# Optimization experiments

Measured on AMD Instinct MI355X. Metric: run time of the kernel, lower is better.

The kernel has to match this reference:

```python
import jax, jax.numpy as jnp
import numpy as np

BASE_T = 0.07
ALPHA = 0.5
EPS = 1e-12  # torch F.normalize eps


def _l2_normalize(x):
    norm = jnp.linalg.norm(x, axis=1, keepdims=True)
    return x / jnp.maximum(norm, EPS)


def setup_inputs() -> dict:
    key = jax.random.key(0)
    k1, k2, k3 = jax.random.split(key, 3)
    B, D, H, W = 4096, 512, 16, 16
    return {
        "emb1": jax.random.normal(k1, (B, D), dtype=jnp.float32),
        "emb2": jax.random.normal(k2, (B, D), dtype=jnp.float32),
        "attention_map": jax.random.uniform(k3, (B, H, W), dtype=jnp.float32),
    }


def reference(emb1, emb2, attention_map):
    B = emb1.shape[0]
    e1 = _l2_normalize(emb1)
    e2 = _l2_normalize(emb2)

    att = attention_map.mean(axis=(1, 2))                     # [B]
    temp = (BASE_T * (1.0 + ALPHA * att))[:, None]            # [B, 1]

    x = jnp.concatenate([e1, e2], axis=0)                     # [2B, D]
    x_swap = jnp.concatenate([e2, e1], axis=0)                # [2B, D]
    temp_cat = jnp.concatenate([temp, temp], axis=0)          # [2B, 1]

    sim = jnp.matmul(x, x.T) / temp_cat                       # [2B, 2B]
    pos_sim = jnp.sum(x * x_swap, axis=1) / temp_cat[:, 0]    # [2B]

    diag = jnp.eye(2 * B, dtype=bool)
    sim = jnp.where(diag, -jnp.inf, sim)                      # exp(-inf) = 0

    denominator = jnp.exp(sim).sum(axis=1)                    # [2B]
    loss = -jnp.log(jnp.exp(pos_sim) / denominator)
    return loss.mean()
```

## Files before the change

### kernel.cpp

```cpp
#include <hip/hip_runtime.h>
#include <hip/hip_bf16.h>
#include <math.h>

#define B_ROWS 4096
#define D_DIM 512
#define TWO_B 8192
#define HW_N 256
#define BASE_T 0.07f
#define ALPHA_C 0.5f
#define LOG2E 1.44269504088896340736f

typedef __bf16 v8bf __attribute__((ext_vector_type(8)));
typedef float v4f __attribute__((ext_vector_type(4)));

__device__ __forceinline__ float fast_exp2(float x) {
#if __has_builtin(__builtin_amdgcn_exp2f)
    return __builtin_amdgcn_exp2f(x);
#else
    return exp2f(x);
#endif
}

__global__ __launch_bounds__(256) void prep_kernel(
    const float* __restrict__ emb1, const float* __restrict__ emb2,
    const float* __restrict__ att, __hip_bfloat16* __restrict__ X,
    float* __restrict__ inv_temp, float* __restrict__ pos)
{
    const int b = blockIdx.x;
    const int t = threadIdx.x;
    const float* e1 = emb1 + (size_t)b * D_DIM;
    const float* e2 = emb2 + (size_t)b * D_DIM;
    float a1 = e1[t], c1 = e1[t + 256];
    float a2 = e2[t], c2 = e2[t + 256];
    float av = att[(size_t)b * HW_N + t];
    float s1 = a1 * a1 + c1 * c1;
    float s2 = a2 * a2 + c2 * c2;
    float s12 = a1 * a2 + c1 * c2;
    #pragma unroll
    for (int m = 1; m < 64; m <<= 1) {
        s1  += __shfl_xor(s1, m, 64);
        s2  += __shfl_xor(s2, m, 64);
        s12 += __shfl_xor(s12, m, 64);
        av  += __shfl_xor(av, m, 64);
    }
    __shared__ float red[4][4];
    const int w = t >> 6, lane = t & 63;
    if (lane == 0) { red[w][0] = s1; red[w][1] = s2; red[w][2] = s12; red[w][3] = av; }
    __syncthreads();
    const float T1  = red[0][0] + red[1][0] + red[2][0] + red[3][0];
    const float T2  = red[0][1] + red[1][1] + red[2][1] + red[3][1];
    const float T12 = red[0][2] + red[1][2] + red[2][2] + red[3][2];
    const float Ta  = red[0][3] + red[1][3] + red[2][3] + red[3][3];
    const float i1 = 1.0f / fmaxf(sqrtf(T1), 1e-12f);
    const float i2 = 1.0f / fmaxf(sqrtf(T2), 1e-12f);
    const float it = 1.0f / (BASE_T * (1.0f + ALPHA_C * (Ta * (1.0f / 256.0f))));
    __hip_bfloat16* x1 = X + (size_t)b * D_DIM;
    __hip_bfloat16* x2 = X + (size_t)(b + B_ROWS) * D_DIM;
    x1[t]       = __float2bfloat16(a1 * i1);
    x1[t + 256] = __float2bfloat16(c1 * i1);
    x2[t]       = __float2bfloat16(a2 * i2);
    x2[t + 256] = __float2bfloat16(c2 * i2);
    if (t == 0) {
        inv_temp[b] = it * LOG2E;
        inv_temp[b + B_ROWS] = it * LOG2E;
        pos[b] = (T12 * i1 * i2) * it;
    }
}

__device__ __forceinline__ void gload_lds16(const void* g, void* s) {
    __builtin_amdgcn_global_load_lds(
        (const __attribute__((address_space(1))) unsigned int*)g,
        (__attribute__((address_space(3))) unsigned int*)s,
        16, 0, 0);
}

__global__ __launch_bounds__(256) void gram_kernel(
    const __hip_bfloat16* __restrict__ X,
    const float* __restrict__ inv_temp,
    float* __restrict__ partial)
{
    const int bid = blockIdx.x;
    int rb = (int)((129.0f - sqrtf(129.0f * 129.0f - 8.0f * (float)bid)) * 0.5f);
    rb = rb < 0 ? 0 : (rb > 63 ? 63 : rb);
    while (rb > 0 && (rb * (129 - rb)) / 2 > bid) rb--;
    while (rb < 63 && ((rb + 1) * (129 - (rb + 1))) / 2 <= bid) rb++;
    const int cb = rb + (bid - (rb * (129 - rb)) / 2);

    __shared__ __hip_bfloat16 smA[128 * 128];
    __shared__ __hip_bfloat16 smB[128 * 128];

    const int rowBase = rb * 128;
    const int colBase = cb * 128;

    const int tid  = threadIdx.x;
    const int w    = tid >> 6;
    const int lane = tid & 63;
    const int quad = lane >> 4;
    const int t    = lane & 15;
    const int wm   = w >> 1;
    const int wn   = w & 1;

    const int srow   = lane >> 4;
    const int schunk = lane & 15;

    v4f acc[4][4];
    #pragma unroll
    for (int a = 0; a < 4; a++)
        #pragma unroll
        for (int b2 = 0; b2 < 4; b2++)
            acc[a][b2] = v4f{0.0f, 0.0f, 0.0f, 0.0f};

    const __hip_bfloat16* Arow0 = X + (size_t)rowBase * D_DIM;
    const __hip_bfloat16* Brow0 = X + (size_t)colBase * D_DIM;

    for (int kk = 0; kk < D_DIM; kk += 128) {
        #pragma unroll
        for (int j = 0; j < 8; j++) {
            const int g = w * 8 + j;
            const int r = g * 4 + srow;
            const int gc = schunk ^ (r & 15);
            gload_lds16(Arow0 + (size_t)r * D_DIM + kk + gc * 8,
                        &smA[g * 512]);
            gload_lds16(Brow0 + (size_t)r * D_DIM + kk + gc * 8,
                        &smB[g * 512]);
        }
        __syncthreads();

        #pragma unroll
        for (int s = 0; s < 4; s++) {
            v8bf af[4], bf[4];
            #pragma unroll
            for (int mi = 0; mi < 4; mi++) {
                const int row = wm * 64 + mi * 16 + t;
                const int p = (s * 4 + quad) ^ t;
                af[mi] = *(const v8bf*)&smA[row * 128 + p * 8];
            }
            #pragma unroll
            for (int ni = 0; ni < 4; ni++) {
                const int col = wn * 64 + ni * 16 + t;
                const int p = (s * 4 + quad) ^ t;
                bf[ni] = *(const v8bf*)&smB[col * 128 + p * 8];
            }
            #pragma unroll
            for (int mi = 0; mi < 4; mi++)
                #pragma unroll
                for (int ni = 0; ni < 4; ni++)
                    acc[mi][ni] = __builtin_amdgcn_mfma_f32_16x16x32_bf16(
                        af[mi], bf[ni], acc[mi][ni], 0, 0, 0);
        }
        __syncthreads();
    }

    v4f itv[4];
    #pragma unroll
    for (int mi = 0; mi < 4; mi++)
        itv[mi] = *(const v4f*)&inv_temp[rowBase + wm * 64 + mi * 16 + quad * 4];

    float* prow = partial + (size_t)(cb * 2 + wn) * TWO_B;
    #pragma unroll
    for (int mi = 0; mi < 4; mi++) {
        #pragma unroll
        for (int r = 0; r < 4; r++) {
            const int i = rowBase + wm * 64 + mi * 16 + quad * 4 + r;
            const float it = itv[mi][r];
            float s = 0.0f;
            #pragma unroll
            for (int ni = 0; ni < 4; ni++) {
                const int j = colBase + wn * 64 + ni * 16 + t;
                const float v = fast_exp2(acc[mi][ni][r] * it);
                s += (i == j) ? 0.0f : v;
            }
            s += __shfl_xor(s, 1, 64);
            s += __shfl_xor(s, 2, 64);
            s += __shfl_xor(s, 4, 64);
            s += __shfl_xor(s, 8, 64);
            if (t == 0) prow[i] = s;
        }
    }

    if (rb != cb) {
        float itj[4];
        float cs[4] = {0.0f, 0.0f, 0.0f, 0.0f};
        #pragma unroll
        for (int ni = 0; ni < 4; ni++)
            itj[ni] = inv_temp[colBase + wn * 64 + ni * 16 + t];
        #pragma unroll
        for (int mi = 0; mi < 4; mi++)
            #pragma unroll
            for (int r = 0; r < 4; r++)
                #pragma unroll
                for (int ni = 0; ni < 4; ni++)
                    cs[ni] += fast_exp2(acc[mi][ni][r] * itj[ni]);
        float* pcol = partial + (size_t)(rb * 2 + wm) * TWO_B;
        #pragma unroll
        for (int ni = 0; ni < 4; ni++) {
            cs[ni] += __shfl_xor(cs[ni], 16, 64);
            cs[ni] += __shfl_xor(cs[ni], 32, 64);
            if (quad == 0) pcol[colBase + wn * 64 + ni * 16 + t] = cs[ni];
        }
    }
}

__global__ __launch_bounds__(256) void finish1(
    const float* __restrict__ partial, const float* __restrict__ pos,
    float* __restrict__ blockSums)
{
    const int i = blockIdx.x * 256 + threadIdx.x;
    float d = 0.0f;
    #pragma unroll 8
    for (int s = 0; s < 128; s++) d += partial[(size_t)s * TWO_B + i];
    float li = logf(d) - pos[i & (B_ROWS - 1)];
    #pragma unroll
    for (int m = 1; m < 64; m <<= 1) li += __shfl_xor(li, m, 64);
    __shared__ float red[4];
    const int w = threadIdx.x >> 6, lane = threadIdx.x & 63;
    if (lane == 0) red[w] = li;
    __syncthreads();
    if (threadIdx.x == 0) blockSums[blockIdx.x] = red[0] + red[1] + red[2] + red[3];
}

__global__ void finish2(const float* __restrict__ blockSums, float* __restrict__ out)
{
    const int lane = threadIdx.x;
    float v = (lane < 32) ? blockSums[lane] : 0.0f;
    #pragma unroll
    for (int m = 1; m < 64; m <<= 1) v += __shfl_xor(v, m, 64);
    if (lane == 0) out[0] = v * (1.0f / 8192.0f);
}

extern "C" void kernel_launch(void* const* d_in, const int* in_sizes, int n_in,
                              void* d_out, int out_size, void* d_ws, size_t ws_size,
                              hipStream_t stream) {
    const float* emb1 = (const float*)d_in[0];
    const float* emb2 = (const float*)d_in[1];
    const float* att  = (const float*)d_in[2];
    float* out = (float*)d_out;

    char* ws = (char*)d_ws;
    __hip_bfloat16* X  = (__hip_bfloat16*)ws;
    float* inv_temp    = (float*)(ws + 8388608);
    float* pos         = (float*)(ws + 8388608 + 32768);
    float* partial     = (float*)(ws + 8388608 + 32768 + 16384);
    float* blockSums   = (float*)(ws + 8388608 + 32768 + 16384 + 4194304);

    prep_kernel<<<B_ROWS, 256, 0, stream>>>(emb1, emb2, att, X, inv_temp, pos);
    gram_kernel<<<2080, 256, 0, stream>>>(X, inv_temp, partial);
    finish1<<<TWO_B / 256, 256, 0, stream>>>(partial, pos, blockSums);
    finish2<<<1, 64, 0, stream>>>(blockSums, out);
}
```

Before: 143.4 us.

## Switch Gram matrix to FP8 MFMA with FP8 normalized embeddings

Normalized embeddings are now stored as packed FP8 instead of bf16, which halves workspace traffic, and the Gram kernel uses fp8 16x16x32 MFMA instructions with 256-byte K tiles, so there are two K iterations instead of four. The prep kernel loads float2 per thread, and the gram block index is permuted across groups of eight for a different schedule over the triangular tiles. The aim is to cut memory and MFMA cost, at the price of much lower precision in the similarity logits. Those logits are divided by a temperature near 0.07 and exponentiated, so the loss may drift from the reference.

```diff
diff --git a/kernel.cpp b/kernel.cpp
--- a/kernel.cpp
+++ b/kernel.cpp
@@ -10,7 +10,6 @@
 #define ALPHA_C 0.5f
 #define LOG2E 1.44269504088896340736f
 
-typedef __bf16 v8bf __attribute__((ext_vector_type(8)));
 typedef float v4f __attribute__((ext_vector_type(4)));
 
 __device__ __forceinline__ float fast_exp2(float x) {
@@ -23,19 +22,17 @@
 
 __global__ __launch_bounds__(256) void prep_kernel(
     const float* __restrict__ emb1, const float* __restrict__ emb2,
-    const float* __restrict__ att, __hip_bfloat16* __restrict__ X,
+    const float* __restrict__ att, unsigned short* __restrict__ X8,
     float* __restrict__ inv_temp, float* __restrict__ pos)
 {
     const int b = blockIdx.x;
     const int t = threadIdx.x;
-    const float* e1 = emb1 + (size_t)b * D_DIM;
-    const float* e2 = emb2 + (size_t)b * D_DIM;
-    float a1 = e1[t], c1 = e1[t + 256];
-    float a2 = e2[t], c2 = e2[t + 256];
+    const float2 a1 = ((const float2*)(emb1 + (size_t)b * D_DIM))[t];
+    const float2 a2 = ((const float2*)(emb2 + (size_t)b * D_DIM))[t];
     float av = att[(size_t)b * HW_N + t];
-    float s1 = a1 * a1 + c1 * c1;
-    float s2 = a2 * a2 + c2 * c2;
-    float s12 = a1 * a2 + c1 * c2;
+    float s1  = a1.x * a1.x + a1.y * a1.y;
+    float s2  = a2.x * a2.x + a2.y * a2.y;
+    float s12 = a1.x * a2.x + a1.y * a2.y;
     #pragma unroll
     for (int m = 1; m < 64; m <<= 1) {
         s1  += __shfl_xor(s1, m, 64);
@@ -54,12 +51,10 @@
     const float i1 = 1.0f / fmaxf(sqrtf(T1), 1e-12f);
     const float i2 = 1.0f / fmaxf(sqrtf(T2), 1e-12f);
     const float it = 1.0f / (BASE_T * (1.0f + ALPHA_C * (Ta * (1.0f / 256.0f))));
-    __hip_bfloat16* x1 = X + (size_t)b * D_DIM;
-    __hip_bfloat16* x2 = X + (size_t)(b + B_ROWS) * D_DIM;
-    x1[t]       = __float2bfloat16(a1 * i1);
-    x1[t + 256] = __float2bfloat16(c1 * i1);
-    x2[t]       = __float2bfloat16(a2 * i2);
-    x2[t + 256] = __float2bfloat16(c2 * i2);
+    const int p1 = __builtin_amdgcn_cvt_pk_fp8_f32(a1.x * i1, a1.y * i1, 0, false);
+    const int p2 = __builtin_amdgcn_cvt_pk_fp8_f32(a2.x * i2, a2.y * i2, 0, false);
+    X8[(size_t)b * 256 + t]            = (unsigned short)(p1 & 0xffff);
+    X8[(size_t)(b + B_ROWS) * 256 + t] = (unsigned short)(p2 & 0xffff);
     if (t == 0) {
         inv_temp[b] = it * LOG2E;
         inv_temp[b + B_ROWS] = it * LOG2E;
@@ -75,19 +70,19 @@
 }
 
 __global__ __launch_bounds__(256) void gram_kernel(
-    const __hip_bfloat16* __restrict__ X,
+    const unsigned char* __restrict__ X8,
     const float* __restrict__ inv_temp,
     float* __restrict__ partial)
 {
-    const int bid = blockIdx.x;
+    const int bid = (blockIdx.x & 7) * 260 + (blockIdx.x >> 3);
     int rb = (int)((129.0f - sqrtf(129.0f * 129.0f - 8.0f * (float)bid)) * 0.5f);
     rb = rb < 0 ? 0 : (rb > 63 ? 63 : rb);
     while (rb > 0 && (rb * (129 - rb)) / 2 > bid) rb--;
     while (rb < 63 && ((rb + 1) * (129 - (rb + 1))) / 2 <= bid) rb++;
     const int cb = rb + (bid - (rb * (129 - rb)) / 2);
 
-    __shared__ __hip_bfloat16 smA[128 * 128];
-    __shared__ __hip_bfloat16 smB[128 * 128];
+    __shared__ unsigned char smA[128 * 256];
+    __shared__ unsigned char smB[128 * 256];
 
     const int rowBase = rb * 128;
     const int colBase = cb * 128;
@@ -103,6 +98,9 @@
     const int srow   = lane >> 4;
     const int schunk = lane & 15;
 
+    const unsigned char* Arow0 = X8 + (size_t)rowBase * D_DIM;
+    const unsigned char* Brow0 = X8 + (size_t)colBase * D_DIM;
+
     v4f acc[4][4];
     #pragma unroll
     for (int a = 0; a < 4; a++)
@@ -110,45 +108,37 @@
         for (int b2 = 0; b2 < 4; b2++)
             acc[a][b2] = v4f{0.0f, 0.0f, 0.0f, 0.0f};
 
-    const __hip_bfloat16* Arow0 = X + (size_t)rowBase * D_DIM;
-    const __hip_bfloat16* Brow0 = X + (size_t)colBase * D_DIM;
-
-    for (int kk = 0; kk < D_DIM; kk += 128) {
+    for (int p = 0; p < 2; p++) {
+        const int kk = p * 256;
         #pragma unroll
         for (int j = 0; j < 8; j++) {
             const int g = w * 8 + j;
             const int r = g * 4 + srow;
             const int gc = schunk ^ (r & 15);
-            gload_lds16(Arow0 + (size_t)r * D_DIM + kk + gc * 8,
-                        &smA[g * 512]);
-            gload_lds16(Brow0 + (size_t)r * D_DIM + kk + gc * 8,
-                        &smB[g * 512]);
+            gload_lds16(Arow0 + (size_t)r * D_DIM + kk + gc * 16, &smA[g * 1024]);
+            gload_lds16(Brow0 + (size_t)r * D_DIM + kk + gc * 16, &smB[g * 1024]);
         }
         __syncthreads();
 
         #pragma unroll
-        for (int s = 0; s < 4; s++) {
-            v8bf af[4], bf[4];
-            #pragma unroll
-            for (int mi = 0; mi < 4; mi++) {
-                const int row = wm * 64 + mi * 16 + t;
-                const int p = (s * 4 + quad) ^ t;
-                af[mi] = *(const v8bf*)&smA[row * 128 + p * 8];
-            }
-            #pragma unroll
-            for (int ni = 0; ni < 4; ni++) {
-                const int col = wn * 64 + ni * 16 + t;
-                const int p = (s * 4 + quad) ^ t;
-                bf[ni] = *(const v8bf*)&smB[col * 128 + p * 8];
-            }
+        for (int s = 0; s < 8; s++) {
+            const int pu = (s * 2 + (quad >> 1)) ^ t;
+            const int off = pu * 16 + (quad & 1) * 8;
+            long aF[4], bF[4];
+            #pragma unroll
+            for (int mi = 0; mi < 4; mi++)
+                aF[mi] = *(const long*)&smA[(wm * 64 + mi * 16 + t) * 256 + off];
+            #pragma unroll
+            for (int ni = 0; ni < 4; ni++)
+                bF[ni] = *(const long*)&smB[(wn * 64 + ni * 16 + t) * 256 + off];
             #pragma unroll
             for (int mi = 0; mi < 4; mi++)
                 #pragma unroll
                 for (int ni = 0; ni < 4; ni++)
-                    acc[mi][ni] = __builtin_amdgcn_mfma_f32_16x16x32_bf16(
-                        af[mi], bf[ni], acc[mi][ni], 0, 0, 0);
-        }
-        __syncthreads();
+                    acc[mi][ni] = __builtin_amdgcn_mfma_f32_16x16x32_fp8_fp8(
+                        aF[mi], bF[ni], acc[mi][ni], 0, 0, 0);
+        }
+        if (p == 0) __syncthreads();
     }
 
     v4f itv[4];
@@ -237,14 +227,14 @@
     float* out = (float*)d_out;
 
     char* ws = (char*)d_ws;
-    __hip_bfloat16* X  = (__hip_bfloat16*)ws;
-    float* inv_temp    = (float*)(ws + 8388608);
-    float* pos         = (float*)(ws + 8388608 + 32768);
-    float* partial     = (float*)(ws + 8388608 + 32768 + 16384);
-    float* blockSums   = (float*)(ws + 8388608 + 32768 + 16384 + 4194304);
-
-    prep_kernel<<<B_ROWS, 256, 0, stream>>>(emb1, emb2, att, X, inv_temp, pos);
-    gram_kernel<<<2080, 256, 0, stream>>>(X, inv_temp, partial);
+    unsigned short* X8 = (unsigned short*)ws;
+    float* inv_temp    = (float*)(ws + 4194304);
+    float* pos         = (float*)(ws + 4194304 + 32768);
+    float* partial     = (float*)(ws + 4194304 + 32768 + 16384);
+    float* blockSums   = (float*)(ws + 4194304 + 32768 + 16384 + 4194304);
+
+    prep_kernel<<<B_ROWS, 256, 0, stream>>>(emb1, emb2, att, X8, inv_temp, pos);
+    gram_kernel<<<2080, 256, 0, stream>>>((const unsigned char*)X8, inv_temp, partial);
     finish1<<<TWO_B / 256, 256, 0, stream>>>(partial, pos, blockSums);
     finish2<<<1, 64, 0, stream>>>(blockSums, out);
 }
```

After: 129.0 us. 1.11x faster.
